# Performance work log

Measured on AMD Instinct MI355X. Metric: run time of the kernel, lower is better.

The kernel has to match this reference:

```python
import jax, jax.numpy as jnp
import numpy as np

EPS = 1e-5
NEG_SLOPE = 0.01


def _bn(h, gamma, beta):
    # Training-mode batch norm over axis 0 (biased variance, like torch)
    m = h.mean(axis=0)
    v = h.var(axis=0)
    return (h - m) * jax.lax.rsqrt(v + EPS) * gamma + beta


def setup_inputs() -> dict:
    N, F, H, C = 2048, 64, 128, 2
    key = jax.random.key(0)
    ks = jax.random.split(key, 12)
    g = lambda k, shp: jax.random.normal(k, shp, dtype=jnp.float32) * 0.05
    return {
        "x": jax.random.normal(ks[0], (N, F), dtype=jnp.float32),
        "node_features": jax.random.uniform(ks[1], (N, F), dtype=jnp.float32),
        "W1": g(ks[2], (F, H)), "b1": jnp.zeros((H,), jnp.float32),
        "g1": jnp.ones((H,), jnp.float32), "be1": jnp.zeros((H,), jnp.float32),
        "W2": g(ks[3], (H, H)), "b2": jnp.zeros((H,), jnp.float32),
        "g2": jnp.ones((H,), jnp.float32), "be2": jnp.zeros((H,), jnp.float32),
        "W3": g(ks[4], (H, F)), "b3": jnp.zeros((F,), jnp.float32),
        "W5": g(ks[5], (F, H)), "b5": jnp.zeros((H,), jnp.float32),
        "g5": jnp.ones((H,), jnp.float32), "be5": jnp.zeros((H,), jnp.float32),
        "W6": g(ks[6], (H, C)), "b6": jnp.zeros((C,), jnp.float32),
    }


def reference(x, node_features, W1, b1, g1, be1, W2, b2, g2, be2, W3, b3,
              W5, b5, g5, be5, W6, b6):
    N = node_features.shape[0]
    C = W6.shape[1]
    # static upper-triangular edge list == torch.combinations(arange(N), r=2)
    ei, ej = np.triu_indices(N, k=1)

    h = node_features
    xinit = h
    h = _bn(jax.nn.leaky_relu(h @ W1 + b1, NEG_SLOPE), g1, be1)
    h = _bn(jax.nn.leaky_relu(h @ W2 + b2, NEG_SLOPE), g2, be2)
    h = h @ W3 + b3 + xinit  # [N, F]

    # edge prediction: gather pairs, elementwise mult, MLP+BN+softmax
    e = h[ei] * h[ej]  # [E, F]
    e = _bn(jax.nn.leaky_relu(e @ W5 + b5, NEG_SLOPE), g5, be5)
    edge_pred = jax.nn.softmax(e @ W6 + b6, axis=-1)  # [E, C]

    probs = jnp.zeros((N, N, C), dtype=edge_pred.dtype)
    probs = probs.at[ei, ej].set(edge_pred).at[ej, ei].set(edge_pred)
    return probs
```

## Files before the change

### kernel.cpp

```cpp
#include <hip/hip_runtime.h>
#include <hip/hip_bf16.h>


typedef short short8 __attribute__((ext_vector_type(8)));
typedef float floatx4 __attribute__((ext_vector_type(4)));
typedef float float2v __attribute__((ext_vector_type(2)));

#define NN 2048
#define EPSV 1e-5f
#define EDGEF 2096128.f

__device__ __forceinline__ float bf2f(short s) {
    return __uint_as_float(((unsigned)(unsigned short)s) << 16);
}
__device__ __forceinline__ short f2bf(float f) {
    unsigned u = __float_as_uint(f);
    unsigned r = (u + 0x7FFFu + ((u >> 16) & 1u)) >> 16;
    return (short)r;
}
__device__ __forceinline__ float lrelu(float x) { return fmaxf(x, 0.01f * x); }

__device__ __forceinline__ unsigned cvt_pk_bf16(float a, float b) {
    unsigned r;
    asm("v_cvt_pk_bf16_f32 %0, %1, %2" : "=v"(r) : "v"(a), "v"(b));
    return r;
}

__device__ __forceinline__ int physB(int h, int f) {
    return ((((h >> 4) * 2 + (f >> 5)) * 64 + ((f >> 3) & 3) * 16 + (h & 15)) * 8) + (f & 7);
}

__device__ __forceinline__ void decode2(int bid, int& i0, int& j0, bool& str) {
    int q = (int)(0.25f * (130.f - sqrtf(16900.f - 8.f * (float)bid)));
    if (q < 0) q = 0;
    while (q > 0 && 130 * q - 2 * q * q > bid) --q;
    while (130 * (q + 1) - 2 * (q + 1) * (q + 1) <= bid) ++q;
    int r = bid - (130 * q - 2 * q * q);
    int n = 32 - q;
    int gs = (r >= n) + (r >= 2 * n) + (r >= 3 * n);
    int g = 4 * q + gs;
    int s = r - gs * n;
    i0 = g * 16;
    j0 = (q + s) * 64;
    str = (s == 0);
}

__global__ __launch_bounds__(256) void k_l1(const float* __restrict__ nf,
                                            const float* __restrict__ W1,
                                            const float* __restrict__ b1,
                                            const float* __restrict__ W5,
                                            float* __restrict__ act1,
                                            float* __restrict__ stat1,
                                            short* __restrict__ w5bf) {
    __shared__ float xl[8 * 64];
    __shared__ float sS[128], sQ[128];
    int t = threadIdx.x, n0 = blockIdx.x * 8;
    if (blockIdx.x < 32) {
        int idx = blockIdx.x * 256 + t;
        w5bf[physB(idx & 127, idx >> 7)] = f2bf(W5[idx]);
    }
    if (t < 128) { sS[t] = 0.f; sQ[t] = 0.f; }
    xl[t] = nf[(size_t)n0 * 64 + t];
    xl[t + 256] = nf[(size_t)n0 * 64 + t + 256];
    __syncthreads();
    int nl = t >> 5, h0 = (t & 31) * 4;
    float acc[4];
    for (int k = 0; k < 4; ++k) acc[k] = b1[h0 + k];
    for (int f = 0; f < 64; ++f) {
        float r = xl[nl * 64 + f];
        const float* wr = W1 + f * 128 + h0;
        for (int k = 0; k < 4; ++k) acc[k] = fmaf(r, wr[k], acc[k]);
    }
    for (int k = 0; k < 4; ++k) {
        float a = lrelu(acc[k]);
        act1[(size_t)(n0 + nl) * 128 + h0 + k] = a;
        atomicAdd(&sS[h0 + k], a);
        atomicAdd(&sQ[h0 + k], a * a);
    }
    __syncthreads();
    if (t < 128) atomicAdd(&stat1[t], sS[t]);
    else atomicAdd(&stat1[t], sQ[t - 128]);
}

__global__ __launch_bounds__(256) void k_l2(const float* __restrict__ act1,
                                            const float* __restrict__ stat1,
                                            const float* __restrict__ g1,
                                            const float* __restrict__ be1,
                                            const float* __restrict__ W2,
                                            const float* __restrict__ b2,
                                            float* __restrict__ act2,
                                            float* __restrict__ stat2) {
    __shared__ float a1n[8 * 128];
    __shared__ float sS[128], sQ[128];
    int t = threadIdx.x, n0 = blockIdx.x * 8;
    if (t < 128) { sS[t] = 0.f; sQ[t] = 0.f; }
    for (int k = 0; k < 4; ++k) {
        int e = t + 256 * k;
        int nl = e >> 7, h = e & 127;
        float m = stat1[h] * (1.f / 2048.f);
        float v = stat1[128 + h] * (1.f / 2048.f) - m * m;
        float sc = rsqrtf(v + EPSV);
        a1n[e] = (act1[(size_t)(n0 + nl) * 128 + h] - m) * sc * g1[h] + be1[h];
    }
    __syncthreads();
    int nl = t >> 5, h0 = (t & 31) * 4;
    float acc[4];
    for (int k = 0; k < 4; ++k) acc[k] = b2[h0 + k];
    for (int hi = 0; hi < 128; ++hi) {
        float r = a1n[nl * 128 + hi];
        const float* wr = W2 + hi * 128 + h0;
        for (int k = 0; k < 4; ++k) acc[k] = fmaf(r, wr[k], acc[k]);
    }
    for (int k = 0; k < 4; ++k) {
        float a = lrelu(acc[k]);
        act2[(size_t)(n0 + nl) * 128 + h0 + k] = a;
        atomicAdd(&sS[h0 + k], a);
        atomicAdd(&sQ[h0 + k], a * a);
    }
    __syncthreads();
    if (t < 128) atomicAdd(&stat2[t], sS[t]);
    else atomicAdd(&stat2[t], sQ[t - 128]);
}

__global__ __launch_bounds__(256) void k_l3(const float* __restrict__ act2,
                                            const float* __restrict__ stat2,
                                            const float* __restrict__ g2,
                                            const float* __restrict__ be2,
                                            const float* __restrict__ W3,
                                            const float* __restrict__ b3,
                                            const float* __restrict__ nf,
                                            short* __restrict__ hb,
                                            float* __restrict__ hf) {
    __shared__ float a2n[8 * 128];
    int t = threadIdx.x, n0 = blockIdx.x * 8;
    for (int k = 0; k < 4; ++k) {
        int e = t + 256 * k;
        int nl = e >> 7, h = e & 127;
        float m = stat2[h] * (1.f / 2048.f);
        float v = stat2[128 + h] * (1.f / 2048.f) - m * m;
        float sc = rsqrtf(v + EPSV);
        a2n[e] = (act2[(size_t)(n0 + nl) * 128 + h] - m) * sc * g2[h] + be2[h];
    }
    __syncthreads();
    int nl = t >> 5, f0 = (t & 31) * 2;
    float acc[2] = {0.f, 0.f};
    for (int hi = 0; hi < 128; ++hi) {
        float r = a2n[nl * 128 + hi];
        const float* wr = W3 + hi * 64 + f0;
        acc[0] = fmaf(r, wr[0], acc[0]);
        acc[1] = fmaf(r, wr[1], acc[1]);
    }
    float v0 = acc[0] + b3[f0] + nf[(size_t)(n0 + nl) * 64 + f0];
    float v1 = acc[1] + b3[f0 + 1] + nf[(size_t)(n0 + nl) * 64 + f0 + 1];
    unsigned p = (unsigned)(unsigned short)f2bf(v0) |
                 ((unsigned)(unsigned short)f2bf(v1) << 16);
    ((unsigned*)hb)[(size_t)(n0 + nl) * 32 + (f0 >> 1)] = p;
    hf[(size_t)(n0 + nl) * 64 + f0] = v0;
    hf[(size_t)(n0 + nl) * 64 + f0 + 1] = v1;
}

__global__ __launch_bounds__(256, 3) void edge_p1(
    const short* __restrict__ hb, const float* __restrict__ hf,
    const short* __restrict__ w5bf, const float* __restrict__ b5,
    float* __restrict__ SQe8)
{
    __shared__ __align__(16) float hi[16 * 64];
    __shared__ __align__(16) short w5s[8192];
    int i0, j0; bool str;
    decode2(blockIdx.x, i0, j0, str);
    int t = threadIdx.x, lane = t & 63, w = t >> 6;
    int quad = lane >> 4, col = lane & 15;

    ((float4*)hi)[t] = ((const float4*)(hf + (size_t)i0 * 64))[t];
#pragma unroll
    for (int k = 0; k < 4; ++k)
        ((float4*)w5s)[t + 256 * k] = ((const float4*)w5bf)[t + 256 * k];

    float hjf[2][8];
#pragma unroll
    for (int ks = 0; ks < 2; ++ks) {
        short8 hv = *(const short8*)(hb + (size_t)(j0 + w * 16 + col) * 64 + ks * 32 + quad * 8);
#pragma unroll
        for (int e = 0; e < 8; ++e) hjf[ks][e] = bf2f(hv[e]);
    }
    float b5v[8];
#pragma unroll
    for (int n = 0; n < 8; ++n) b5v[n] = b5[n * 16 + col];

    float S[8], Q[8];
#pragma unroll
    for (int n = 0; n < 8; ++n) { S[n] = 0.f; Q[n] = 0.f; }
    floatx4 zero4 = {0.f, 0.f, 0.f, 0.f};

    const short* w5w = w5s + (size_t)lane * 8;

    __syncthreads();

    auto mkfrag = [&](int il, short8 (&af)[2]) {
#pragma unroll
        for (int ks = 0; ks < 2; ++ks) {
            const float* hp = &hi[il * 64 + ks * 32 + quad * 8];
            float4 h0 = *(const float4*)hp;
            float4 h1 = *(const float4*)(hp + 4);
            int4 aw;
            aw.x = cvt_pk_bf16(h0.x * hjf[ks][0], h0.y * hjf[ks][1]);
            aw.y = cvt_pk_bf16(h0.z * hjf[ks][2], h0.w * hjf[ks][3]);
            aw.z = cvt_pk_bf16(h1.x * hjf[ks][4], h1.y * hjf[ks][5]);
            aw.w = cvt_pk_bf16(h1.z * hjf[ks][6], h1.w * hjf[ks][7]);
            af[ks] = *(short8*)&aw;
        }
    };

    if (!str) {
#pragma unroll 2
        for (int il = 0; il < 16; ++il) {
            short8 af[2];
            mkfrag(il, af);
#pragma unroll
            for (int n = 0; n < 8; ++n) {
                short8 wv0 = *(const short8*)(w5w + n * 1024);
                short8 wv1 = *(const short8*)(w5w + n * 1024 + 512);
                floatx4 c = __builtin_amdgcn_mfma_f32_16x16x32_bf16(af[0], wv0, zero4, 0, 0, 0);
                c = __builtin_amdgcn_mfma_f32_16x16x32_bf16(af[1], wv1, c, 0, 0, 0);
                float b = b5v[n];
#pragma unroll
                for (int r = 0; r < 4; ++r) {
                    float a = lrelu(c[r] + b);
                    S[n] += a;
                    Q[n] = fmaf(a, a, Q[n]);
                }
            }
        }
    } else {
        int jgb = j0 + w * 16 + quad * 4;
#pragma unroll 2
        for (int il = 0; il < 16; ++il) {
            short8 af[2];
            mkfrag(il, af);
            int ig = i0 + il;
#pragma unroll
            for (int n = 0; n < 8; ++n) {
                short8 wv0 = *(const short8*)(w5w + n * 1024);
                short8 wv1 = *(const short8*)(w5w + n * 1024 + 512);
                floatx4 c = __builtin_amdgcn_mfma_f32_16x16x32_bf16(af[0], wv0, zero4, 0, 0, 0);
                c = __builtin_amdgcn_mfma_f32_16x16x32_bf16(af[1], wv1, c, 0, 0, 0);
                float b = b5v[n];
#pragma unroll
                for (int r = 0; r < 4; ++r) {
                    float a = (jgb + r > ig) ? lrelu(c[r] + b) : 0.f;
                    S[n] += a;
                    Q[n] = fmaf(a, a, Q[n]);
                }
            }
        }
    }

    float* dst = SQe8 + (blockIdx.x & 7) * 256;
#pragma unroll
    for (int n = 0; n < 8; ++n) {
        float Sa = S[n], Qa = Q[n];
        Sa += __shfl_xor(Sa, 16); Sa += __shfl_xor(Sa, 32);
        Qa += __shfl_xor(Qa, 16); Qa += __shfl_xor(Qa, 32);
        if (quad == 0) {
            atomicAdd(&dst[n * 16 + col], Sa);
            atomicAdd(&dst[128 + n * 16 + col], Qa);
        }
    }
}

__global__ __launch_bounds__(256, 3) void edge_p2(
    const short* __restrict__ hb, const float* __restrict__ hf,
    const short* __restrict__ w5bf, const float* __restrict__ b5,
    const float* __restrict__ SQe8, const float* __restrict__ W6,
    const float* __restrict__ b6, const float* __restrict__ g5,
    const float* __restrict__ be5, float* __restrict__ out)
{
    __shared__ __align__(16) float hi[16 * 64];
    __shared__ __align__(16) short w5s[8192];
    __shared__ __align__(16) float sw6[128];
    __shared__ float sred[2];
    __shared__ float sp[16][65];
    int i0, j0; bool str;
    decode2(blockIdx.x, i0, j0, str);
    int t = threadIdx.x, lane = t & 63, w = t >> 6;
    int quad = lane >> 4, col = lane & 15;

    ((float4*)hi)[t] = ((const float4*)(hf + (size_t)i0 * 64))[t];
#pragma unroll
    for (int k = 0; k < 4; ++k)
        ((float4*)w5s)[t + 256 * k] = ((const float4*)w5bf)[t + 256 * k];

    float partv = 0.f;
    if (t < 128) {
        float s = 0.f, q = 0.f;
#pragma unroll
        for (int x = 0; x < 8; ++x) {
            s += SQe8[x * 256 + t];
            q += SQe8[x * 256 + 128 + t];
        }
        float m = s * (1.f / EDGEF);
        float v = q * (1.f / EDGEF) - m * m;
        float sc = rsqrtf(v + EPSV);
        float dW = W6[t * 2] - W6[t * 2 + 1];
        float sg = sc * g5[t];
        sw6[t] = sg * dW;
        partv = (be5[t] - m * sg) * dW;
    }
#pragma unroll
    for (int d = 1; d < 64; d <<= 1) partv += __shfl_xor(partv, d);
    if (t < 128 && lane == 0) sred[w] = partv;

    float hjf[2][8];
#pragma unroll
    for (int ks = 0; ks < 2; ++ks) {
        short8 hv = *(const short8*)(hb + (size_t)(j0 + w * 16 + col) * 64 + ks * 32 + quad * 8);
#pragma unroll
        for (int e = 0; e < 8; ++e) hjf[ks][e] = bf2f(hv[e]);
    }
    floatx4 b5q4[8];
#pragma unroll
    for (int n = 0; n < 8; ++n)
        b5q4[n] = *(const floatx4*)(b5 + n * 16 + quad * 4);

    const short* w5w = w5s + (size_t)lane * 8;

    __syncthreads();
    float bb = b6[0] - b6[1] + sred[0] + sred[1];
    floatx4 w6q4[8];
#pragma unroll
    for (int n = 0; n < 8; ++n)
        w6q4[n] = *(const floatx4*)&sw6[n * 16 + quad * 4];
    floatx4 zero4 = {0.f, 0.f, 0.f, 0.f};

    auto mkfrag = [&](int il, short8 (&af)[2]) {
#pragma unroll
        for (int ks = 0; ks < 2; ++ks) {
            const float* hp = &hi[il * 64 + ks * 32 + quad * 8];
            float4 h0 = *(const float4*)hp;
            float4 h1 = *(const float4*)(hp + 4);
            int4 aw;
            aw.x = cvt_pk_bf16(h0.x * hjf[ks][0], h0.y * hjf[ks][1]);
            aw.y = cvt_pk_bf16(h0.z * hjf[ks][2], h0.w * hjf[ks][3]);
            aw.z = cvt_pk_bf16(h1.x * hjf[ks][4], h1.y * hjf[ks][5]);
            aw.w = cvt_pk_bf16(h1.z * hjf[ks][6], h1.w * hjf[ks][7]);
            af[ks] = *(short8*)&aw;
        }
    };

#pragma unroll 2
    for (int il = 0; il < 16; ++il) {
        short8 af[2];
        mkfrag(il, af);
        float va[4] = {0.f, 0.f, 0.f, 0.f};
#pragma unroll
        for (int n = 0; n < 8; ++n) {
            short8 wv0 = *(const short8*)(w5w + n * 1024);
            short8 wv1 = *(const short8*)(w5w + n * 1024 + 512);
            floatx4 c = __builtin_amdgcn_mfma_f32_16x16x32_bf16(wv0, af[0], zero4, 0, 0, 0);
            c = __builtin_amdgcn_mfma_f32_16x16x32_bf16(wv1, af[1], c, 0, 0, 0);
#pragma unroll
            for (int r = 0; r < 4; ++r)
                va[r] = fmaf(lrelu(c[r] + ((const float*)&b5q4[n])[r]),
                             ((const float*)&w6q4[n])[r], va[r]);
        }
        float v = (va[0] + va[1]) + (va[2] + va[3]);
        v += __shfl_xor(v, 16);
        v += __shfl_xor(v, 32);
        v += bb;
        float p = 1.f / (1.f + __expf(-v));
        if (quad == 0) sp[il][w * 16 + col] = p;
    }
    __syncthreads();

    if (!str) {
        int il = t >> 4, jb = (t & 15) * 4;
        float* op = out + ((size_t)(i0 + il) * NN + j0 + jb) * 2;
#pragma unroll
        for (int q2 = 0; q2 < 2; ++q2) {
            float p0 = sp[il][jb + q2 * 2], p1 = sp[il][jb + q2 * 2 + 1];
            float4 u; u.x = p0; u.y = 1.f - p0; u.z = p1; u.w = 1.f - p1;
            *(float4*)(op + q2 * 4) = u;
        }
        int jl = t >> 2, ib = (t & 3) * 4;
        float* om = out + ((size_t)(j0 + jl) * NN + i0 + ib) * 2;
#pragma unroll
        for (int q2 = 0; q2 < 2; ++q2) {
            float p0 = sp[ib + q2 * 2][jl], p1 = sp[ib + q2 * 2 + 1][jl];
            float4 u; u.x = p0; u.y = 1.f - p0; u.z = p1; u.w = 1.f - p1;
            *(float4*)(om + q2 * 4) = u;
        }
    } else {
        int il = t >> 4, jb = (t & 15) * 4;
        int ig = i0 + il;
#pragma unroll
        for (int e = 0; e < 4; ++e) {
            int jg = j0 + jb + e;
            if (jg > ig) {
                float p = sp[il][jb + e];
                float2v pr; pr.x = p; pr.y = 1.f - p;
                *(float2v*)(out + ((size_t)ig * NN + jg) * 2) = pr;
            } else if (jg == ig) {
                float2v pr; pr.x = 0.f; pr.y = 0.f;
                *(float2v*)(out + ((size_t)ig * NN + jg) * 2) = pr;
            }
        }
        int jl = t >> 2, ib = (t & 3) * 4;
        int jg = j0 + jl;
#pragma unroll
        for (int e = 0; e < 4; ++e) {
            int ig2 = i0 + ib + e;
            if (jg > ig2) {
                float p = sp[ib + e][jl];
                float2v pr; pr.x = p; pr.y = 1.f - p;
                *(float2v*)(out + ((size_t)jg * NN + ig2) * 2) = pr;
            }
        }
    }
}

extern "C" void kernel_launch(void* const* d_in, const int* in_sizes, int n_in,
                              void* d_out, int out_size, void* d_ws, size_t ws_size,
                              hipStream_t stream) {
    const float* nf  = (const float*)d_in[1];
    const float* W1  = (const float*)d_in[2];
    const float* b1  = (const float*)d_in[3];
    const float* g1  = (const float*)d_in[4];
    const float* be1 = (const float*)d_in[5];
    const float* W2  = (const float*)d_in[6];
    const float* b2  = (const float*)d_in[7];
    const float* g2  = (const float*)d_in[8];
    const float* be2 = (const float*)d_in[9];
    const float* W3  = (const float*)d_in[10];
    const float* b3  = (const float*)d_in[11];
    const float* W5  = (const float*)d_in[12];
    const float* b5  = (const float*)d_in[13];
    const float* g5  = (const float*)d_in[14];
    const float* be5 = (const float*)d_in[15];
    const float* W6  = (const float*)d_in[16];
    const float* b6  = (const float*)d_in[17];
    float* out = (float*)d_out;

    float* wsf   = (float*)d_ws;
    float* stat1 = wsf;
    float* stat2 = wsf + 256;
    float* SQe8  = wsf + 512;
    float* act1  = wsf + 4096;
    float* act2  = act1 + 262144;
    short* hb    = (short*)(act2 + 262144);
    short* w5bf  = hb + 131072;
    float* hf    = (float*)(w5bf + 8192);

    hipMemsetAsync(d_ws, 0, 4096 * sizeof(float), stream);

    k_l1<<<256, 256, 0, stream>>>(nf, W1, b1, W5, act1, stat1, w5bf);
    k_l2<<<256, 256, 0, stream>>>(act1, stat1, g1, be1, W2, b2, act2, stat2);
    k_l3<<<256, 256, 0, stream>>>(act2, stat2, g2, be2, W3, b3, nf, hb, hf);

    edge_p1<<<2112, 256, 0, stream>>>(hb, hf, w5bf, b5, SQe8);
    edge_p2<<<2112, 256, 0, stream>>>(hb, hf, w5bf, b5, SQe8, W6, b6, g5, be5, out);
}
```

Baseline: 244.8 us.

## Fuse node MLP and edge passes into persistent kernels with grid barriers

Merges the three node-layer kernels into one kernel that keeps activations in shared memory and uses atomic-counter grid barriers for the batch-norm statistics. The two edge passes become one persistent kernel of 704 blocks that loops over tiles, with a grid barrier between the statistics pass and the output pass. This removes launch gaps and the act1/act2 global round trips. It relies on every block being co-resident, which risks deadlock if occupancy is lower than assumed, and the spin barriers add their own synchronisation cost.

```diff
diff --git a/kernel.cpp b/kernel.cpp
--- a/kernel.cpp
+++ b/kernel.cpp
@@ -9,6 +9,7 @@
 #define NN 2048
 #define EPSV 1e-5f
 #define EDGEF 2096128.f
+#define EGRID 704
 
 __device__ __forceinline__ float bf2f(short s) {
     return __uint_as_float(((unsigned)(unsigned short)s) << 16);
@@ -45,374 +46,376 @@
     str = (s == 0);
 }
 
-__global__ __launch_bounds__(256) void k_l1(const float* __restrict__ nf,
-                                            const float* __restrict__ W1,
-                                            const float* __restrict__ b1,
-                                            const float* __restrict__ W5,
-                                            float* __restrict__ act1,
-                                            float* __restrict__ stat1,
-                                            short* __restrict__ w5bf) {
-    __shared__ float xl[8 * 64];
+__device__ __forceinline__ void gbar(int* ctr, int target) {
+    __threadfence();
+    __syncthreads();
+    if (threadIdx.x == 0) {
+        atomicAdd(ctr, 1);
+        while (atomicAdd(ctr, 0) < target) {}
+    }
+    __syncthreads();
+    __threadfence();
+}
+
+__global__ __launch_bounds__(256) void k_nodes(
+    const float* __restrict__ nf,
+    const float* __restrict__ W1, const float* __restrict__ b1,
+    const float* __restrict__ g1, const float* __restrict__ be1,
+    const float* __restrict__ W2, const float* __restrict__ b2,
+    const float* __restrict__ g2, const float* __restrict__ be2,
+    const float* __restrict__ W3, const float* __restrict__ b3,
+    const float* __restrict__ W5,
+    float* __restrict__ stat1, float* __restrict__ stat2,
+    int* __restrict__ bars,
+    short* __restrict__ w5bf, short* __restrict__ hb, float* __restrict__ hf)
+{
+    __shared__ float A[8 * 128];
+    __shared__ float B[8 * 128];
     __shared__ float sS[128], sQ[128];
     int t = threadIdx.x, n0 = blockIdx.x * 8;
+
     if (blockIdx.x < 32) {
         int idx = blockIdx.x * 256 + t;
         w5bf[physB(idx & 127, idx >> 7)] = f2bf(W5[idx]);
     }
+
     if (t < 128) { sS[t] = 0.f; sQ[t] = 0.f; }
-    xl[t] = nf[(size_t)n0 * 64 + t];
-    xl[t + 256] = nf[(size_t)n0 * 64 + t + 256];
+    B[t] = nf[(size_t)n0 * 64 + t];
+    B[t + 256] = nf[(size_t)n0 * 64 + t + 256];
     __syncthreads();
     int nl = t >> 5, h0 = (t & 31) * 4;
-    float acc[4];
-    for (int k = 0; k < 4; ++k) acc[k] = b1[h0 + k];
-    for (int f = 0; f < 64; ++f) {
-        float r = xl[nl * 64 + f];
-        const float* wr = W1 + f * 128 + h0;
-        for (int k = 0; k < 4; ++k) acc[k] = fmaf(r, wr[k], acc[k]);
-    }
-    for (int k = 0; k < 4; ++k) {
-        float a = lrelu(acc[k]);
-        act1[(size_t)(n0 + nl) * 128 + h0 + k] = a;
-        atomicAdd(&sS[h0 + k], a);
-        atomicAdd(&sQ[h0 + k], a * a);
+    {
+        float acc[4];
+        for (int k = 0; k < 4; ++k) acc[k] = b1[h0 + k];
+        for (int f = 0; f < 64; ++f) {
+            float r = B[nl * 64 + f];
+            const float* wr = W1 + f * 128 + h0;
+            for (int k = 0; k < 4; ++k) acc[k] = fmaf(r, wr[k], acc[k]);
+        }
+        for (int k = 0; k < 4; ++k) {
+            float a = lrelu(acc[k]);
+            A[nl * 128 + h0 + k] = a;
+            atomicAdd(&sS[h0 + k], a);
+            atomicAdd(&sQ[h0 + k], a * a);
+        }
     }
     __syncthreads();
     if (t < 128) atomicAdd(&stat1[t], sS[t]);
     else atomicAdd(&stat1[t], sQ[t - 128]);
-}
-
-__global__ __launch_bounds__(256) void k_l2(const float* __restrict__ act1,
-                                            const float* __restrict__ stat1,
-                                            const float* __restrict__ g1,
-                                            const float* __restrict__ be1,
-                                            const float* __restrict__ W2,
-                                            const float* __restrict__ b2,
-                                            float* __restrict__ act2,
-                                            float* __restrict__ stat2) {
-    __shared__ float a1n[8 * 128];
-    __shared__ float sS[128], sQ[128];
-    int t = threadIdx.x, n0 = blockIdx.x * 8;
+
+    gbar(bars + 0, 256);
+
     if (t < 128) { sS[t] = 0.f; sQ[t] = 0.f; }
     for (int k = 0; k < 4; ++k) {
         int e = t + 256 * k;
-        int nl = e >> 7, h = e & 127;
+        int h = e & 127;
         float m = stat1[h] * (1.f / 2048.f);
         float v = stat1[128 + h] * (1.f / 2048.f) - m * m;
         float sc = rsqrtf(v + EPSV);
-        a1n[e] = (act1[(size_t)(n0 + nl) * 128 + h] - m) * sc * g1[h] + be1[h];
-    }
-    __syncthreads();
-    int nl = t >> 5, h0 = (t & 31) * 4;
-    float acc[4];
-    for (int k = 0; k < 4; ++k) acc[k] = b2[h0 + k];
-    for (int hi = 0; hi < 128; ++hi) {
-        float r = a1n[nl * 128 + hi];
-        const float* wr = W2 + hi * 128 + h0;
-        for (int k = 0; k < 4; ++k) acc[k] = fmaf(r, wr[k], acc[k]);
-    }
-    for (int k = 0; k < 4; ++k) {
-        float a = lrelu(acc[k]);
-        act2[(size_t)(n0 + nl) * 128 + h0 + k] = a;
-        atomicAdd(&sS[h0 + k], a);
-        atomicAdd(&sQ[h0 + k], a * a);
+        B[e] = (A[e] - m) * sc * g1[h] + be1[h];
+    }
+    __syncthreads();
+    {
+        float acc[4];
+        for (int k = 0; k < 4; ++k) acc[k] = b2[h0 + k];
+        for (int hi = 0; hi < 128; ++hi) {
+            float r = B[nl * 128 + hi];
+            const float* wr = W2 + hi * 128 + h0;
+            for (int k = 0; k < 4; ++k) acc[k] = fmaf(r, wr[k], acc[k]);
+        }
+        __syncthreads();
+        for (int k = 0; k < 4; ++k) {
+            float a = lrelu(acc[k]);
+            A[nl * 128 + h0 + k] = a;
+            atomicAdd(&sS[h0 + k], a);
+            atomicAdd(&sQ[h0 + k], a * a);
+        }
     }
     __syncthreads();
     if (t < 128) atomicAdd(&stat2[t], sS[t]);
     else atomicAdd(&stat2[t], sQ[t - 128]);
-}
-
-__global__ __launch_bounds__(256) void k_l3(const float* __restrict__ act2,
-                                            const float* __restrict__ stat2,
-                                            const float* __restrict__ g2,
-                                            const float* __restrict__ be2,
-                                            const float* __restrict__ W3,
-                                            const float* __restrict__ b3,
-                                            const float* __restrict__ nf,
-                                            short* __restrict__ hb,
-                                            float* __restrict__ hf) {
-    __shared__ float a2n[8 * 128];
-    int t = threadIdx.x, n0 = blockIdx.x * 8;
+
+    gbar(bars + 1, 256);
+
     for (int k = 0; k < 4; ++k) {
         int e = t + 256 * k;
-        int nl = e >> 7, h = e & 127;
+        int h = e & 127;
         float m = stat2[h] * (1.f / 2048.f);
         float v = stat2[128 + h] * (1.f / 2048.f) - m * m;
         float sc = rsqrtf(v + EPSV);
-        a2n[e] = (act2[(size_t)(n0 + nl) * 128 + h] - m) * sc * g2[h] + be2[h];
-    }
-    __syncthreads();
-    int nl = t >> 5, f0 = (t & 31) * 2;
-    float acc[2] = {0.f, 0.f};
-    for (int hi = 0; hi < 128; ++hi) {
-        float r = a2n[nl * 128 + hi];
-        const float* wr = W3 + hi * 64 + f0;
-        acc[0] = fmaf(r, wr[0], acc[0]);
-        acc[1] = fmaf(r, wr[1], acc[1]);
-    }
-    float v0 = acc[0] + b3[f0] + nf[(size_t)(n0 + nl) * 64 + f0];
-    float v1 = acc[1] + b3[f0 + 1] + nf[(size_t)(n0 + nl) * 64 + f0 + 1];
-    unsigned p = (unsigned)(unsigned short)f2bf(v0) |
-                 ((unsigned)(unsigned short)f2bf(v1) << 16);
-    ((unsigned*)hb)[(size_t)(n0 + nl) * 32 + (f0 >> 1)] = p;
-    hf[(size_t)(n0 + nl) * 64 + f0] = v0;
-    hf[(size_t)(n0 + nl) * 64 + f0 + 1] = v1;
-}
-
-__global__ __launch_bounds__(256, 3) void edge_p1(
+        B[e] = (A[e] - m) * sc * g2[h] + be2[h];
+    }
+    __syncthreads();
+    {
+        int f0 = (t & 31) * 2;
+        float acc0 = 0.f, acc1 = 0.f;
+        for (int hi = 0; hi < 128; ++hi) {
+            float r = B[nl * 128 + hi];
+            const float* wr = W3 + hi * 64 + f0;
+            acc0 = fmaf(r, wr[0], acc0);
+            acc1 = fmaf(r, wr[1], acc1);
+        }
+        float v0 = acc0 + b3[f0] + nf[(size_t)(n0 + nl) * 64 + f0];
+        float v1 = acc1 + b3[f0 + 1] + nf[(size_t)(n0 + nl) * 64 + f0 + 1];
+        unsigned p = (unsigned)(unsigned short)f2bf(v0) |
+                     ((unsigned)(unsigned short)f2bf(v1) << 16);
+        ((unsigned*)hb)[(size_t)(n0 + nl) * 32 + (f0 >> 1)] = p;
+        hf[(size_t)(n0 + nl) * 64 + f0] = v0;
+        hf[(size_t)(n0 + nl) * 64 + f0 + 1] = v1;
+    }
+}
+
+__global__ __launch_bounds__(256, 3) void k_edges(
     const short* __restrict__ hb, const float* __restrict__ hf,
     const short* __restrict__ w5bf, const float* __restrict__ b5,
-    float* __restrict__ SQe8)
-{
-    __shared__ __align__(16) float hi[16 * 64];
-    __shared__ __align__(16) short w5s[8192];
-    int i0, j0; bool str;
-    decode2(blockIdx.x, i0, j0, str);
-    int t = threadIdx.x, lane = t & 63, w = t >> 6;
-    int quad = lane >> 4, col = lane & 15;
-
-    ((float4*)hi)[t] = ((const float4*)(hf + (size_t)i0 * 64))[t];
-#pragma unroll
-    for (int k = 0; k < 4; ++k)
-        ((float4*)w5s)[t + 256 * k] = ((const float4*)w5bf)[t + 256 * k];
-
-    float hjf[2][8];
-#pragma unroll
-    for (int ks = 0; ks < 2; ++ks) {
-        short8 hv = *(const short8*)(hb + (size_t)(j0 + w * 16 + col) * 64 + ks * 32 + quad * 8);
-#pragma unroll
-        for (int e = 0; e < 8; ++e) hjf[ks][e] = bf2f(hv[e]);
-    }
-    float b5v[8];
-#pragma unroll
-    for (int n = 0; n < 8; ++n) b5v[n] = b5[n * 16 + col];
-
-    float S[8], Q[8];
-#pragma unroll
-    for (int n = 0; n < 8; ++n) { S[n] = 0.f; Q[n] = 0.f; }
-    floatx4 zero4 = {0.f, 0.f, 0.f, 0.f};
-
-    const short* w5w = w5s + (size_t)lane * 8;
-
-    __syncthreads();
-
-    auto mkfrag = [&](int il, short8 (&af)[2]) {
-#pragma unroll
-        for (int ks = 0; ks < 2; ++ks) {
-            const float* hp = &hi[il * 64 + ks * 32 + quad * 8];
-            float4 h0 = *(const float4*)hp;
-            float4 h1 = *(const float4*)(hp + 4);
-            int4 aw;
-            aw.x = cvt_pk_bf16(h0.x * hjf[ks][0], h0.y * hjf[ks][1]);
-            aw.y = cvt_pk_bf16(h0.z * hjf[ks][2], h0.w * hjf[ks][3]);
-            aw.z = cvt_pk_bf16(h1.x * hjf[ks][4], h1.y * hjf[ks][5]);
-            aw.w = cvt_pk_bf16(h1.z * hjf[ks][6], h1.w * hjf[ks][7]);
-            af[ks] = *(short8*)&aw;
-        }
-    };
-
-    if (!str) {
-#pragma unroll 2
-        for (int il = 0; il < 16; ++il) {
-            short8 af[2];
-            mkfrag(il, af);
-#pragma unroll
-            for (int n = 0; n < 8; ++n) {
-                short8 wv0 = *(const short8*)(w5w + n * 1024);
-                short8 wv1 = *(const short8*)(w5w + n * 1024 + 512);
-                floatx4 c = __builtin_amdgcn_mfma_f32_16x16x32_bf16(af[0], wv0, zero4, 0, 0, 0);
-                c = __builtin_amdgcn_mfma_f32_16x16x32_bf16(af[1], wv1, c, 0, 0, 0);
-                float b = b5v[n];
-#pragma unroll
-                for (int r = 0; r < 4; ++r) {
-                    float a = lrelu(c[r] + b);
-                    S[n] += a;
-                    Q[n] = fmaf(a, a, Q[n]);
-                }
-            }
-        }
-    } else {
-        int jgb = j0 + w * 16 + quad * 4;
-#pragma unroll 2
-        for (int il = 0; il < 16; ++il) {
-            short8 af[2];
-            mkfrag(il, af);
-            int ig = i0 + il;
-#pragma unroll
-            for (int n = 0; n < 8; ++n) {
-                short8 wv0 = *(const short8*)(w5w + n * 1024);
-                short8 wv1 = *(const short8*)(w5w + n * 1024 + 512);
-                floatx4 c = __builtin_amdgcn_mfma_f32_16x16x32_bf16(af[0], wv0, zero4, 0, 0, 0);
-                c = __builtin_amdgcn_mfma_f32_16x16x32_bf16(af[1], wv1, c, 0, 0, 0);
-                float b = b5v[n];
-#pragma unroll
-                for (int r = 0; r < 4; ++r) {
-                    float a = (jgb + r > ig) ? lrelu(c[r] + b) : 0.f;
-                    S[n] += a;
-                    Q[n] = fmaf(a, a, Q[n]);
-                }
-            }
-        }
-    }
-
-    float* dst = SQe8 + (blockIdx.x & 7) * 256;
-#pragma unroll
-    for (int n = 0; n < 8; ++n) {
-        float Sa = S[n], Qa = Q[n];
-        Sa += __shfl_xor(Sa, 16); Sa += __shfl_xor(Sa, 32);
-        Qa += __shfl_xor(Qa, 16); Qa += __shfl_xor(Qa, 32);
-        if (quad == 0) {
-            atomicAdd(&dst[n * 16 + col], Sa);
-            atomicAdd(&dst[128 + n * 16 + col], Qa);
-        }
-    }
-}
-
-__global__ __launch_bounds__(256, 3) void edge_p2(
-    const short* __restrict__ hb, const float* __restrict__ hf,
-    const short* __restrict__ w5bf, const float* __restrict__ b5,
-    const float* __restrict__ SQe8, const float* __restrict__ W6,
+    float* __restrict__ SQe8, const float* __restrict__ W6,
     const float* __restrict__ b6, const float* __restrict__ g5,
-    const float* __restrict__ be5, float* __restrict__ out)
+    const float* __restrict__ be5, int* __restrict__ bars,
+    float* __restrict__ out)
 {
     __shared__ __align__(16) float hi[16 * 64];
     __shared__ __align__(16) short w5s[8192];
     __shared__ __align__(16) float sw6[128];
     __shared__ float sred[2];
     __shared__ float sp[16][65];
-    int i0, j0; bool str;
-    decode2(blockIdx.x, i0, j0, str);
+
     int t = threadIdx.x, lane = t & 63, w = t >> 6;
     int quad = lane >> 4, col = lane & 15;
 
-    ((float4*)hi)[t] = ((const float4*)(hf + (size_t)i0 * 64))[t];
 #pragma unroll
     for (int k = 0; k < 4; ++k)
         ((float4*)w5s)[t + 256 * k] = ((const float4*)w5bf)[t + 256 * k];
-
-    float partv = 0.f;
-    if (t < 128) {
-        float s = 0.f, q = 0.f;
-#pragma unroll
-        for (int x = 0; x < 8; ++x) {
-            s += SQe8[x * 256 + t];
-            q += SQe8[x * 256 + 128 + t];
-        }
-        float m = s * (1.f / EDGEF);
-        float v = q * (1.f / EDGEF) - m * m;
-        float sc = rsqrtf(v + EPSV);
-        float dW = W6[t * 2] - W6[t * 2 + 1];
-        float sg = sc * g5[t];
-        sw6[t] = sg * dW;
-        partv = (be5[t] - m * sg) * dW;
-    }
-#pragma unroll
-    for (int d = 1; d < 64; d <<= 1) partv += __shfl_xor(partv, d);
-    if (t < 128 && lane == 0) sred[w] = partv;
-
-    float hjf[2][8];
-#pragma unroll
-    for (int ks = 0; ks < 2; ++ks) {
-        short8 hv = *(const short8*)(hb + (size_t)(j0 + w * 16 + col) * 64 + ks * 32 + quad * 8);
-#pragma unroll
-        for (int e = 0; e < 8; ++e) hjf[ks][e] = bf2f(hv[e]);
-    }
-    floatx4 b5q4[8];
-#pragma unroll
-    for (int n = 0; n < 8; ++n)
-        b5q4[n] = *(const floatx4*)(b5 + n * 16 + quad * 4);
-
     const short* w5w = w5s + (size_t)lane * 8;
-
-    __syncthreads();
-    float bb = b6[0] - b6[1] + sred[0] + sred[1];
-    floatx4 w6q4[8];
-#pragma unroll
-    for (int n = 0; n < 8; ++n)
-        w6q4[n] = *(const floatx4*)&sw6[n * 16 + quad * 4];
     floatx4 zero4 = {0.f, 0.f, 0.f, 0.f};
 
-    auto mkfrag = [&](int il, short8 (&af)[2]) {
-#pragma unroll
-        for (int ks = 0; ks < 2; ++ks) {
-            const float* hp = &hi[il * 64 + ks * 32 + quad * 8];
-            float4 h0 = *(const float4*)hp;
-            float4 h1 = *(const float4*)(hp + 4);
-            int4 aw;
-            aw.x = cvt_pk_bf16(h0.x * hjf[ks][0], h0.y * hjf[ks][1]);
-            aw.y = cvt_pk_bf16(h0.z * hjf[ks][2], h0.w * hjf[ks][3]);
-            aw.z = cvt_pk_bf16(h1.x * hjf[ks][4], h1.y * hjf[ks][5]);
-            aw.w = cvt_pk_bf16(h1.z * hjf[ks][6], h1.w * hjf[ks][7]);
-            af[ks] = *(short8*)&aw;
-        }
-    };
-
+    {
+        float b5v[8];
+#pragma unroll
+        for (int n = 0; n < 8; ++n) b5v[n] = b5[n * 16 + col];
+        float S[8], Q[8];
+#pragma unroll
+        for (int n = 0; n < 8; ++n) { S[n] = 0.f; Q[n] = 0.f; }
+
+#pragma unroll 1
+        for (int tile = blockIdx.x; tile < 2112; tile += EGRID) {
+            int i0, j0; bool str;
+            decode2(tile, i0, j0, str);
+            __syncthreads();
+            ((float4*)hi)[t] = ((const float4*)(hf + (size_t)i0 * 64))[t];
+            float hjf[2][8];
+#pragma unroll
+            for (int ks = 0; ks < 2; ++ks) {
+                short8 hv = *(const short8*)(hb + (size_t)(j0 + w * 16 + col) * 64 + ks * 32 + quad * 8);
+#pragma unroll
+                for (int e = 0; e < 8; ++e) hjf[ks][e] = bf2f(hv[e]);
+            }
+            __syncthreads();
+
+            auto mkfrag = [&](int il, short8 (&af)[2]) {
+#pragma unroll
+                for (int ks = 0; ks < 2; ++ks) {
+                    const float* hp = &hi[il * 64 + ks * 32 + quad * 8];
+                    float4 h0 = *(const float4*)hp;
+                    float4 h1 = *(const float4*)(hp + 4);
+                    int4 aw;
+                    aw.x = cvt_pk_bf16(h0.x * hjf[ks][0], h0.y * hjf[ks][1]);
+                    aw.y = cvt_pk_bf16(h0.z * hjf[ks][2], h0.w * hjf[ks][3]);
+                    aw.z = cvt_pk_bf16(h1.x * hjf[ks][4], h1.y * hjf[ks][5]);
+                    aw.w = cvt_pk_bf16(h1.z * hjf[ks][6], h1.w * hjf[ks][7]);
+                    af[ks] = *(short8*)&aw;
+                }
+            };
+
+            if (!str) {
 #pragma unroll 2
-    for (int il = 0; il < 16; ++il) {
-        short8 af[2];
-        mkfrag(il, af);
-        float va[4] = {0.f, 0.f, 0.f, 0.f};
+                for (int il = 0; il < 16; ++il) {
+                    short8 af[2];
+                    mkfrag(il, af);
+#pragma unroll
+                    for (int n = 0; n < 8; ++n) {
+                        short8 wv0 = *(const short8*)(w5w + n * 1024);
+                        short8 wv1 = *(const short8*)(w5w + n * 1024 + 512);
+                        floatx4 c = __builtin_amdgcn_mfma_f32_16x16x32_bf16(af[0], wv0, zero4, 0, 0, 0);
+                        c = __builtin_amdgcn_mfma_f32_16x16x32_bf16(af[1], wv1, c, 0, 0, 0);
+                        float b = b5v[n];
+#pragma unroll
+                        for (int r = 0; r < 4; ++r) {
+                            float a = lrelu(c[r] + b);
+                            S[n] += a;
+                            Q[n] = fmaf(a, a, Q[n]);
+                        }
+                    }
+                }
+            } else {
+                int jgb = j0 + w * 16 + quad * 4;
+#pragma unroll 2
+                for (int il = 0; il < 16; ++il) {
+                    short8 af[2];
+                    mkfrag(il, af);
+                    int ig = i0 + il;
+#pragma unroll
+                    for (int n = 0; n < 8; ++n) {
+                        short8 wv0 = *(const short8*)(w5w + n * 1024);
+                        short8 wv1 = *(const short8*)(w5w + n * 1024 + 512);
+                        floatx4 c = __builtin_amdgcn_mfma_f32_16x16x32_bf16(af[0], wv0, zero4, 0, 0, 0);
+                        c = __builtin_amdgcn_mfma_f32_16x16x32_bf16(af[1], wv1, c, 0, 0, 0);
+                        float b = b5v[n];
+#pragma unroll
+                        for (int r = 0; r < 4; ++r) {
+                            float a = (jgb + r > ig) ? lrelu(c[r] + b) : 0.f;
+                            S[n] += a;
+                            Q[n] = fmaf(a, a, Q[n]);
+                        }
+                    }
+                }
+            }
+        }
+
+        float* dst = SQe8 + (blockIdx.x & 7) * 256;
 #pragma unroll
         for (int n = 0; n < 8; ++n) {
-            short8 wv0 = *(const short8*)(w5w + n * 1024);
-            short8 wv1 = *(const short8*)(w5w + n * 1024 + 512);
-            floatx4 c = __builtin_amdgcn_mfma_f32_16x16x32_bf16(wv0, af[0], zero4, 0, 0, 0);
-            c = __builtin_amdgcn_mfma_f32_16x16x32_bf16(wv1, af[1], c, 0, 0, 0);
-#pragma unroll
-            for (int r = 0; r < 4; ++r)
-                va[r] = fmaf(lrelu(c[r] + ((const float*)&b5q4[n])[r]),
-                             ((const float*)&w6q4[n])[r], va[r]);
-        }
-        float v = (va[0] + va[1]) + (va[2] + va[3]);
-        v += __shfl_xor(v, 16);
-        v += __shfl_xor(v, 32);
-        v += bb;
-        float p = 1.f / (1.f + __expf(-v));
-        if (quad == 0) sp[il][w * 16 + col] = p;
-    }
-    __syncthreads();
-
-    if (!str) {
-        int il = t >> 4, jb = (t & 15) * 4;
-        float* op = out + ((size_t)(i0 + il) * NN + j0 + jb) * 2;
-#pragma unroll
-        for (int q2 = 0; q2 < 2; ++q2) {
-            float p0 = sp[il][jb + q2 * 2], p1 = sp[il][jb + q2 * 2 + 1];
-            float4 u; u.x = p0; u.y = 1.f - p0; u.z = p1; u.w = 1.f - p1;
-            *(float4*)(op + q2 * 4) = u;
-        }
-        int jl = t >> 2, ib = (t & 3) * 4;
-        float* om = out + ((size_t)(j0 + jl) * NN + i0 + ib) * 2;
-#pragma unroll
-        for (int q2 = 0; q2 < 2; ++q2) {
-            float p0 = sp[ib + q2 * 2][jl], p1 = sp[ib + q2 * 2 + 1][jl];
-            float4 u; u.x = p0; u.y = 1.f - p0; u.z = p1; u.w = 1.f - p1;
-            *(float4*)(om + q2 * 4) = u;
-        }
-    } else {
-        int il = t >> 4, jb = (t & 15) * 4;
-        int ig = i0 + il;
-#pragma unroll
-        for (int e = 0; e < 4; ++e) {
-            int jg = j0 + jb + e;
-            if (jg > ig) {
-                float p = sp[il][jb + e];
-                float2v pr; pr.x = p; pr.y = 1.f - p;
-                *(float2v*)(out + ((size_t)ig * NN + jg) * 2) = pr;
-            } else if (jg == ig) {
-                float2v pr; pr.x = 0.f; pr.y = 0.f;
-                *(float2v*)(out + ((size_t)ig * NN + jg) * 2) = pr;
-            }
-        }
-        int jl = t >> 2, ib = (t & 3) * 4;
-        int jg = j0 + jl;
-#pragma unroll
-        for (int e = 0; e < 4; ++e) {
-            int ig2 = i0 + ib + e;
-            if (jg > ig2) {
-                float p = sp[ib + e][jl];
-                float2v pr; pr.x = p; pr.y = 1.f - p;
-                *(float2v*)(out + ((size_t)jg * NN + ig2) * 2) = pr;
+            float Sa = S[n], Qa = Q[n];
+            Sa += __shfl_xor(Sa, 16); Sa += __shfl_xor(Sa, 32);
+            Qa += __shfl_xor(Qa, 16); Qa += __shfl_xor(Qa, 32);
+            if (quad == 0) {
+                atomicAdd(&dst[n * 16 + col], Sa);
+                atomicAdd(&dst[128 + n * 16 + col], Qa);
+            }
+        }
+    }
+
+    gbar(bars, EGRID);
+
+    {
+        float partv = 0.f;
+        if (t < 128) {
+            float s = 0.f, q = 0.f;
+#pragma unroll
+            for (int x = 0; x < 8; ++x) {
+                s += SQe8[x * 256 + t];
+                q += SQe8[x * 256 + 128 + t];
+            }
+            float m = s * (1.f / EDGEF);
+            float v = q * (1.f / EDGEF) - m * m;
+            float sc = rsqrtf(v + EPSV);
+            float dW = W6[t * 2] - W6[t * 2 + 1];
+            float sg = sc * g5[t];
+            sw6[t] = sg * dW;
+            partv = (be5[t] - m * sg) * dW;
+        }
+#pragma unroll
+        for (int d = 1; d < 64; d <<= 1) partv += __shfl_xor(partv, d);
+        if (t < 128 && lane == 0) sred[w] = partv;
+    }
+    __syncthreads();
+
+    {
+        float bb = b6[0] - b6[1] + sred[0] + sred[1];
+        floatx4 b5q4[8], w6q4[8];
+#pragma unroll
+        for (int n = 0; n < 8; ++n) {
+            b5q4[n] = *(const floatx4*)(b5 + n * 16 + quad * 4);
+            w6q4[n] = *(const floatx4*)&sw6[n * 16 + quad * 4];
+        }
+
+#pragma unroll 1
+        for (int tile = blockIdx.x; tile < 2112; tile += EGRID) {
+            int i0, j0; bool str;
+            decode2(tile, i0, j0, str);
+            __syncthreads();
+            ((float4*)hi)[t] = ((const float4*)(hf + (size_t)i0 * 64))[t];
+            float hjf[2][8];
+#pragma unroll
+            for (int ks = 0; ks < 2; ++ks) {
+                short8 hv = *(const short8*)(hb + (size_t)(j0 + w * 16 + col) * 64 + ks * 32 + quad * 8);
+#pragma unroll
+                for (int e = 0; e < 8; ++e) hjf[ks][e] = bf2f(hv[e]);
+            }
+            __syncthreads();
+
+            auto mkfrag = [&](int il, short8 (&af)[2]) {
+#pragma unroll
+                for (int ks = 0; ks < 2; ++ks) {
+                    const float* hp = &hi[il * 64 + ks * 32 + quad * 8];
+                    float4 h0 = *(const float4*)hp;
+                    float4 h1 = *(const float4*)(hp + 4);
+                    int4 aw;
+                    aw.x = cvt_pk_bf16(h0.x * hjf[ks][0], h0.y * hjf[ks][1]);
+                    aw.y = cvt_pk_bf16(h0.z * hjf[ks][2], h0.w * hjf[ks][3]);
+                    aw.z = cvt_pk_bf16(h1.x * hjf[ks][4], h1.y * hjf[ks][5]);
+                    aw.w = cvt_pk_bf16(h1.z * hjf[ks][6], h1.w * hjf[ks][7]);
+                    af[ks] = *(short8*)&aw;
+                }
+            };
+
+#pragma unroll 2
+            for (int il = 0; il < 16; ++il) {
+                short8 af[2];
+                mkfrag(il, af);
+                float va[4] = {0.f, 0.f, 0.f, 0.f};
+#pragma unroll
+                for (int n = 0; n < 8; ++n) {
+                    short8 wv0 = *(const short8*)(w5w + n * 1024);
+                    short8 wv1 = *(const short8*)(w5w + n * 1024 + 512);
+                    floatx4 c = __builtin_amdgcn_mfma_f32_16x16x32_bf16(wv0, af[0], zero4, 0, 0, 0);
+                    c = __builtin_amdgcn_mfma_f32_16x16x32_bf16(wv1, af[1], c, 0, 0, 0);
+#pragma unroll
+                    for (int r = 0; r < 4; ++r)
+                        va[r] = fmaf(lrelu(c[r] + ((const float*)&b5q4[n])[r]),
+                                     ((const float*)&w6q4[n])[r], va[r]);
+                }
+                float v = (va[0] + va[1]) + (va[2] + va[3]);
+                v += __shfl_xor(v, 16);
+                v += __shfl_xor(v, 32);
+                v += bb;
+                float p = 1.f / (1.f + __expf(-v));
+                if (quad == 0) sp[il][w * 16 + col] = p;
+            }
+            __syncthreads();
+
+            if (!str) {
+                int il2 = t >> 4, jb = (t & 15) * 4;
+                float* op = out + ((size_t)(i0 + il2) * NN + j0 + jb) * 2;
+#pragma unroll
+                for (int q2 = 0; q2 < 2; ++q2) {
+                    float p0 = sp[il2][jb + q2 * 2], p1 = sp[il2][jb + q2 * 2 + 1];
+                    float4 u; u.x = p0; u.y = 1.f - p0; u.z = p1; u.w = 1.f - p1;
+                    *(float4*)(op + q2 * 4) = u;
+                }
+                int jl = t >> 2, ib = (t & 3) * 4;
+                float* om = out + ((size_t)(j0 + jl) * NN + i0 + ib) * 2;
+#pragma unroll
+                for (int q2 = 0; q2 < 2; ++q2) {
+                    float p0 = sp[ib + q2 * 2][jl], p1 = sp[ib + q2 * 2 + 1][jl];
+                    float4 u; u.x = p0; u.y = 1.f - p0; u.z = p1; u.w = 1.f - p1;
+                    *(float4*)(om + q2 * 4) = u;
+                }
+            } else {
+                int il2 = t >> 4, jb = (t & 15) * 4;
+                int ig = i0 + il2;
+#pragma unroll
+                for (int e = 0; e < 4; ++e) {
+                    int jg = j0 + jb + e;
+                    if (jg > ig) {
+                        float p = sp[il2][jb + e];
+                        float2v pr; pr.x = p; pr.y = 1.f - p;
+                        *(float2v*)(out + ((size_t)ig * NN + jg) * 2) = pr;
+                    } else if (jg == ig) {
+                        float2v pr; pr.x = 0.f; pr.y = 0.f;
+                        *(float2v*)(out + ((size_t)ig * NN + jg) * 2) = pr;
+                    }
+                }
+                int jl = t >> 2, ib = (t & 3) * 4;
+                int jg = j0 + jl;
+#pragma unroll
+                for (int e = 0; e < 4; ++e) {
+                    int ig2 = i0 + ib + e;
+                    if (jg > ig2) {
+                        float p = sp[ib + e][jl];
+                        float2v pr; pr.x = p; pr.y = 1.f - p;
+                        *(float2v*)(out + ((size_t)jg * NN + ig2) * 2) = pr;
+                    }
+                }
             }
         }
     }
@@ -444,18 +447,17 @@
     float* stat1 = wsf;
     float* stat2 = wsf + 256;
     float* SQe8  = wsf + 512;
+    int*   bars  = (int*)(wsf + 2560);
     float* act1  = wsf + 4096;
-    float* act2  = act1 + 262144;
-    short* hb    = (short*)(act2 + 262144);
+    short* hb    = (short*)(act1 + 524288);
     short* w5bf  = hb + 131072;
     float* hf    = (float*)(w5bf + 8192);
 
     hipMemsetAsync(d_ws, 0, 4096 * sizeof(float), stream);
 
-    k_l1<<<256, 256, 0, stream>>>(nf, W1, b1, W5, act1, stat1, w5bf);
-    k_l2<<<256, 256, 0, stream>>>(act1, stat1, g1, be1, W2, b2, act2, stat2);
-    k_l3<<<256, 256, 0, stream>>>(act2, stat2, g2, be2, W3, b3, nf, hb, hf);
-
-    edge_p1<<<2112, 256, 0, stream>>>(hb, hf, w5bf, b5, SQe8);
-    edge_p2<<<2112, 256, 0, stream>>>(hb, hf, w5bf, b5, SQe8, W6, b6, g5, be5, out);
-}
+    k_nodes<<<256, 256, 0, stream>>>(nf, W1, b1, g1, be1, W2, b2, g2, be2,
+                                     W3, b3, W5, stat1, stat2, bars,
+                                     w5bf, hb, hf);
+    k_edges<<<EGRID, 256, 0, stream>>>(hb, hf, w5bf, b5, SQe8, W6, b6, g5,
+                                       be5, bars + 2, out);
+}
```

Result: slower. 454.5 us (+85.7%).
